# Optimization experiments

Measured on AMD Instinct MI355X. Metric: run time of the kernel, lower is better.

The kernel has to match this reference:

```python
import jax, jax.numpy as jnp
import numpy as np


def setup_inputs() -> dict:
    key = jax.random.key(0)
    ks = jax.random.split(key, 8)
    B, L, F, H, A = 128, 196, 2048, 512, 512
    features = jax.random.normal(ks[0], (B, L, F), dtype=jnp.float32)
    hidden_state = jax.random.normal(ks[1], (B, H), dtype=jnp.float32)
    # Linear params (PyTorch layout: weight [out, in], bias [out]); scaled like kaiming-uniform
    W_enc = jax.random.normal(ks[2], (A, F), dtype=jnp.float32) / np.sqrt(F)
    b_enc = jnp.zeros((A,), dtype=jnp.float32)
    W_dec = jax.random.normal(ks[3], (A, H), dtype=jnp.float32) / np.sqrt(H)
    b_dec = jnp.zeros((A,), dtype=jnp.float32)
    W_com = jax.random.normal(ks[4], (1, A), dtype=jnp.float32) / np.sqrt(A)
    b_com = jnp.zeros((1,), dtype=jnp.float32)
    return {
        "features": features, "hidden_state": hidden_state,
        "W_enc": W_enc, "b_enc": b_enc,
        "W_dec": W_dec, "b_dec": b_dec,
        "W_com": W_com, "b_com": b_com,
    }


def reference(features, hidden_state, W_enc, b_enc, W_dec, b_dec, W_com, b_com):
    # encoder_context: [B, L, A]
    enc = jnp.einsum('blf,af->bla', features, W_enc) + b_enc
    # decoder_context: [B, 1, A]
    dec = (hidden_state @ W_dec.T + b_dec)[:, None, :]
    # relu + linear to scalar score (dropout in eval mode = identity): [B, L]
    scores = jnp.einsum('bla,a->bl', jax.nn.relu(enc + dec), W_com[0]) + b_com[0]
    alpha = jax.nn.softmax(scores, axis=1)  # [B, L]
    weighted_features = jnp.einsum('blf,bl->bf', features, alpha)  # [B, F]
    return weighted_features, alpha
```

## Files before the change

### kernel.cpp

```cpp
#include <hip/hip_runtime.h>
#include <hip/hip_bf16.h>
#include <math.h>

#define B_  128
#define L_  196
#define F_  2048
#define H_  512
#define A_  512
#define ML_ (B_*L_)

typedef _Float16 half8 __attribute__((ext_vector_type(8)));
typedef _Float16 half4v __attribute__((ext_vector_type(4)));
typedef float f32x4 __attribute__((ext_vector_type(4)));

__device__ __forceinline__ void gld_lds16(const void* g, void* l) {
  __builtin_amdgcn_global_load_lds((const __attribute__((address_space(1))) void*)g,
                                   (__attribute__((address_space(3))) void*)l, 16, 0, 0);
}

__global__ __launch_bounds__(256) void k_dec(const float* __restrict__ hs,
                                             const float* __restrict__ Wdec,
                                             const float* __restrict__ bdec,
                                             const float* __restrict__ benc,
                                             float* __restrict__ dec,
                                             float* __restrict__ scores) {
  const int b = blockIdx.x, t = threadIdx.x;
  const int g = b * 256 + t;
  if (g < ML_) scores[g] = 0.f;

  __shared__ float h[H_];
  h[t]       = hs[b * H_ + t];
  h[t + 256] = hs[b * H_ + t + 256];
  __syncthreads();

#pragma unroll
  for (int r = 0; r < 2; r++) {
    const int a = t + r * 256;
    float acc = bdec[a] + benc[a];
    const float4* wr = (const float4*)(Wdec + (size_t)a * H_);
#pragma unroll 4
    for (int k4 = 0; k4 < H_ / 4; k4++) {
      const float4 w = wr[k4];
      acc += w.x * h[4*k4] + w.y * h[4*k4+1] + w.z * h[4*k4+2] + w.w * h[4*k4+3];
    }
    dec[b * A_ + a] = acc;
  }
}

__global__ __launch_bounds__(256) void k_cvt(const float4* __restrict__ src,
                                             half4v* __restrict__ dst, int n4) {
  for (int i = blockIdx.x * 256 + threadIdx.x; i < n4; i += gridDim.x * 256) {
    const float4 v = src[i];
    half4v o = { (_Float16)v.x, (_Float16)v.y, (_Float16)v.z, (_Float16)v.w };
    dst[i] = o;
  }
}

__global__ __launch_bounds__(256) void k_scores_mfma(const _Float16* __restrict__ fA,
                                                     const _Float16* __restrict__ fB,
                                                     const float* __restrict__ dec,
                                                     const float* __restrict__ wcom,
                                                     float* __restrict__ scores) {
  __shared__ _Float16 As[128 * 64];
  __shared__ _Float16 Bs[128 * 64];
  __shared__ float decS[2][128];

  const int tid  = threadIdx.x;
  const int lane = tid & 63;
  const int w    = tid >> 6;
  const int a0   = blockIdx.x * 128;
  const int m0   = blockIdx.y * 128;
  const int wm   = w & 1;
  const int wn   = w >> 1;
  const int quad = lane >> 4;
  const int l16  = lane & 15;

  f32x4 acc[4][4];
#pragma unroll
  for (int i = 0; i < 4; i++)
#pragma unroll
    for (int j = 0; j < 4; j++)
#pragma unroll
      for (int k = 0; k < 4; k++) acc[i][j][k] = 0.f;

  const int srow   = lane >> 3;
  const int schunk = (lane & 7) ^ srow;
  const _Float16* gAb = fA + (size_t)(m0 + srow) * F_ + schunk * 8;
  const _Float16* gBb = fB + (size_t)(a0 + srow) * F_ + schunk * 8;

  for (int kt = 0; kt < F_; kt += 64) {
#pragma unroll
    for (int i = 0; i < 4; i++) {
      const int r = w * 32 + i * 8;
      gld_lds16(gAb + (size_t)r * F_ + kt, &As[r * 64]);
      gld_lds16(gBb + (size_t)r * F_ + kt, &Bs[r * 64]);
    }
    __syncthreads();

#pragma unroll
    for (int k32 = 0; k32 < 2; k32++) {
      half8 af[4], bf[4];
#pragma unroll
      for (int mt = 0; mt < 4; mt++) {
        const int row = wm * 64 + mt * 16 + l16;
        const int pos = (k32 * 4 + quad) ^ (row & 7);
        af[mt] = *(const half8*)&As[row * 64 + pos * 8];
      }
#pragma unroll
      for (int at = 0; at < 4; at++) {
        const int row = wn * 64 + at * 16 + l16;
        const int pos = (k32 * 4 + quad) ^ (row & 7);
        bf[at] = *(const half8*)&Bs[row * 64 + pos * 8];
      }
#pragma unroll
      for (int mt = 0; mt < 4; mt++)
#pragma unroll
        for (int at = 0; at < 4; at++)
          acc[mt][at] = __builtin_amdgcn_mfma_f32_16x16x32_f16(af[mt], bf[at], acc[mt][at], 0, 0, 0);
    }
    __syncthreads();
  }

  const int b0 = m0 / L_;
  {
    const int i = tid >> 7;
    const int j = tid & 127;
    int bb = b0 + i; if (bb > B_ - 1) bb = B_ - 1;
    decS[i][j] = dec[bb * A_ + a0 + j];
  }
  __syncthreads();

  float w4[4];
#pragma unroll
  for (int at = 0; at < 4; at++) w4[at] = wcom[a0 + wn * 64 + at * 16 + l16];

#pragma unroll
  for (int mt = 0; mt < 4; mt++) {
#pragma unroll
    for (int r = 0; r < 4; r++) {
      const int m  = m0 + wm * 64 + mt * 16 + quad * 4 + r;
      const int db = m / L_ - b0;
      float p = 0.f;
#pragma unroll
      for (int at = 0; at < 4; at++) {
        const float e = acc[mt][at][r] + decS[db][wn * 64 + at * 16 + l16];
        p = fmaf(fmaxf(e, 0.f), w4[at], p);
      }
      p += __shfl_xor(p, 1);
      p += __shfl_xor(p, 2);
      p += __shfl_xor(p, 4);
      p += __shfl_xor(p, 8);
      if (l16 == 0) atomicAdd(&scores[m], p);
    }
  }
}

__global__ __launch_bounds__(256) void k_scores(const float* __restrict__ feat,
                                                const float* __restrict__ Wenc,
                                                const float* __restrict__ dec,
                                                const float* __restrict__ wcom,
                                                float* __restrict__ scores) {
  __shared__ float As[16][128];
  __shared__ float Bs[16][128];

  const int tid = threadIdx.x;
  const int m0 = blockIdx.x * 128;
  const int a0 = blockIdx.y * 128;
  const int tx = tid & 15;
  const int ty = tid >> 4;

  float acc[8][8];
#pragma unroll
  for (int i = 0; i < 8; i++)
#pragma unroll
    for (int j = 0; j < 8; j++) acc[i][j] = 0.f;

  for (int kt = 0; kt < F_; kt += 16) {
#pragma unroll
    for (int rep = 0; rep < 2; rep++) {
      const int idx = rep * 256 + tid;
      const int row = idx >> 2;
      const int kp  = (idx & 3) << 2;
      const float4 v = *(const float4*)(feat + (size_t)(m0 + row) * F_ + kt + kp);
      As[kp+0][row] = v.x; As[kp+1][row] = v.y; As[kp+2][row] = v.z; As[kp+3][row] = v.w;
      const float4 w = *(const float4*)(Wenc + (size_t)(a0 + row) * F_ + kt + kp);
      Bs[kp+0][row] = w.x; Bs[kp+1][row] = w.y; Bs[kp+2][row] = w.z; Bs[kp+3][row] = w.w;
    }
    __syncthreads();

#pragma unroll
    for (int k = 0; k < 16; k++) {
      float ar[8], br[8];
      *(float4*)&ar[0] = *(const float4*)&As[k][ty * 8];
      *(float4*)&ar[4] = *(const float4*)&As[k][ty * 8 + 4];
      *(float4*)&br[0] = *(const float4*)&Bs[k][tx * 8];
      *(float4*)&br[4] = *(const float4*)&Bs[k][tx * 8 + 4];
#pragma unroll
      for (int i = 0; i < 8; i++)
#pragma unroll
        for (int j = 0; j < 8; j++) acc[i][j] = fmaf(ar[i], br[j], acc[i][j]);
    }
    __syncthreads();
  }

  float w8[8];
  *(float4*)&w8[0] = *(const float4*)(wcom + a0 + tx * 8);
  *(float4*)&w8[4] = *(const float4*)(wcom + a0 + tx * 8 + 4);

#pragma unroll
  for (int i = 0; i < 8; i++) {
    const int m = m0 + ty * 8 + i;
    const int b = m / L_;
    const float* dp = dec + b * A_ + a0 + tx * 8;
    float p = 0.f;
#pragma unroll
    for (int j = 0; j < 8; j++) {
      const float e = acc[i][j] + dp[j];
      p = fmaf(fmaxf(e, 0.f), w8[j], p);
    }
    p += __shfl_xor(p, 1);
    p += __shfl_xor(p, 2);
    p += __shfl_xor(p, 4);
    p += __shfl_xor(p, 8);
    if (tx == 0) atomicAdd(&scores[m], p);
  }
}

__global__ __launch_bounds__(256) void k_softmax(const float* __restrict__ scores,
                                                 float* __restrict__ alpha) {
  const int b = blockIdx.x, t = threadIdx.x;
  __shared__ float redm[4];
  __shared__ float reds[4];

  float s = (t < L_) ? scores[b * L_ + t] : -INFINITY;

  float m = s;
#pragma unroll
  for (int o = 32; o >= 1; o >>= 1) m = fmaxf(m, __shfl_xor(m, o));
  if ((t & 63) == 0) redm[t >> 6] = m;
  __syncthreads();
  m = fmaxf(fmaxf(redm[0], redm[1]), fmaxf(redm[2], redm[3]));

  float e = (t < L_) ? expf(s - m) : 0.f;
  float sum = e;
#pragma unroll
  for (int o = 32; o >= 1; o >>= 1) sum += __shfl_xor(sum, o);
  if ((t & 63) == 0) reds[t >> 6] = sum;
  __syncthreads();
  sum = reds[0] + reds[1] + reds[2] + reds[3];

  if (t < L_) alpha[b * L_ + t] = e / sum;
}

__global__ __launch_bounds__(256) void k_wsum(const float* __restrict__ feat,
                                              const float* __restrict__ alpha,
                                              float* __restrict__ out) {
  const int fc = blockIdx.x;
  const int b  = blockIdx.y;
  const int t  = threadIdx.x;

  __shared__ float al[L_];
  for (int i = t; i < L_; i += 256) al[i] = alpha[b * L_ + i];
  __syncthreads();

  const int f = fc * 256 + t;
  const float* fp = feat + (size_t)b * L_ * F_ + f;
  float acc = 0.f;
#pragma unroll 4
  for (int l = 0; l < L_; l++) acc = fmaf(fp[(size_t)l * F_], al[l], acc);
  out[b * F_ + f] = acc;
}

extern "C" void kernel_launch(void* const* d_in, const int* in_sizes, int n_in,
                              void* d_out, int out_size, void* d_ws, size_t ws_size,
                              hipStream_t stream) {
  const float* feat = (const float*)d_in[0];
  const float* hs   = (const float*)d_in[1];
  const float* Wenc = (const float*)d_in[2];
  const float* benc = (const float*)d_in[3];
  const float* Wdec = (const float*)d_in[4];
  const float* bdec = (const float*)d_in[5];
  const float* wcom = (const float*)d_in[6];

  float* out   = (float*)d_out;
  float* alpha = out + B_ * F_;
  float* dec    = (float*)d_ws;
  float* scores = dec + B_ * A_;

  const size_t need = (size_t)(B_ * A_ + ML_) * 4
                    + ((size_t)ML_ * F_ + (size_t)A_ * F_) * 2;

  k_dec<<<dim3(B_), dim3(256), 0, stream>>>(hs, Wdec, bdec, benc, dec, scores);

  if (ws_size >= need) {
    _Float16* fH = (_Float16*)(scores + ML_);
    _Float16* wH = fH + (size_t)ML_ * F_;
    k_cvt<<<dim3(4096), dim3(256), 0, stream>>>((const float4*)feat, (half4v*)fH, ML_ * F_ / 4);
    k_cvt<<<dim3(256),  dim3(256), 0, stream>>>((const float4*)Wenc, (half4v*)wH, A_ * F_ / 4);
    k_scores_mfma<<<dim3(A_ / 128, ML_ / 128), dim3(256), 0, stream>>>(fH, wH, dec, wcom, scores);
  } else {
    k_scores<<<dim3(ML_ / 128, A_ / 128), dim3(256), 0, stream>>>(feat, Wenc, dec, wcom, scores);
  }

  k_softmax<<<dim3(B_), dim3(256), 0, stream>>>(scores, alpha);
  k_wsum<<<dim3(F_ / 256, B_), dim3(256), 0, stream>>>(feat, alpha, out);
}
```

Measured before the change: 470.4 us.

## Fuse prep kernels, fuse softmax into weighted sum, read fp16 features

The two conversion kernels and the decoder projection are merged into one launch, which removes launch gaps. Softmax is folded into the weighted-sum kernel, and each block recomputes it per batch row. The weighted sum now reads the fp16 copy of the features instead of the fp32 original, which halves that read traffic but makes the output depend on fp16-rounded inputs. The dec tile load in the MFMA kernel is moved ahead of the main loop. The weighted-sum blocks also change from 256 to 512 columns, using 2-wide loads.

```diff
diff --git a/kernel.cpp b/kernel.cpp
--- a/kernel.cpp
+++ b/kernel.cpp
@@ -11,6 +11,7 @@
 
 typedef _Float16 half8 __attribute__((ext_vector_type(8)));
 typedef _Float16 half4v __attribute__((ext_vector_type(4)));
+typedef _Float16 half2v __attribute__((ext_vector_type(2)));
 typedef float f32x4 __attribute__((ext_vector_type(4)));
 
 __device__ __forceinline__ void gld_lds16(const void* g, void* l) {
@@ -18,17 +19,39 @@
                                    (__attribute__((address_space(3))) void*)l, 16, 0, 0);
 }
 
-__global__ __launch_bounds__(256) void k_dec(const float* __restrict__ hs,
-                                             const float* __restrict__ Wdec,
-                                             const float* __restrict__ bdec,
-                                             const float* __restrict__ benc,
-                                             float* __restrict__ dec,
-                                             float* __restrict__ scores) {
-  const int b = blockIdx.x, t = threadIdx.x;
+__global__ __launch_bounds__(256) void k_prep(const float4* __restrict__ feat4,
+                                              half4v* __restrict__ fH,
+                                              const float4* __restrict__ Wenc4,
+                                              half4v* __restrict__ wH,
+                                              const float* __restrict__ hs,
+                                              const float* __restrict__ Wdec,
+                                              const float* __restrict__ bdec,
+                                              const float* __restrict__ benc,
+                                              float* __restrict__ dec,
+                                              float* __restrict__ scores) {
+  __shared__ float h[H_];
+  const int bx = blockIdx.x, t = threadIdx.x;
+
+  if (bx < 4096) {
+    const int n4 = ML_ * F_ / 4;
+    for (int i = bx * 256 + t; i < n4; i += 4096 * 256) {
+      const float4 v = feat4[i];
+      half4v o = { (_Float16)v.x, (_Float16)v.y, (_Float16)v.z, (_Float16)v.w };
+      fH[i] = o;
+    }
+    return;
+  }
+
+  const int b = bx - 4096;
   const int g = b * 256 + t;
   if (g < ML_) scores[g] = 0.f;
 
-  __shared__ float h[H_];
+  for (int i = b * 256 + t; i < A_ * F_ / 4; i += 128 * 256) {
+    const float4 v = Wenc4[i];
+    half4v o = { (_Float16)v.x, (_Float16)v.y, (_Float16)v.z, (_Float16)v.w };
+    wH[i] = o;
+  }
+
   h[t]       = hs[b * H_ + t];
   h[t + 256] = hs[b * H_ + t + 256];
   __syncthreads();
@@ -44,15 +67,6 @@
       acc += w.x * h[4*k4] + w.y * h[4*k4+1] + w.z * h[4*k4+2] + w.w * h[4*k4+3];
     }
     dec[b * A_ + a] = acc;
-  }
-}
-
-__global__ __launch_bounds__(256) void k_cvt(const float4* __restrict__ src,
-                                             half4v* __restrict__ dst, int n4) {
-  for (int i = blockIdx.x * 256 + threadIdx.x; i < n4; i += gridDim.x * 256) {
-    const float4 v = src[i];
-    half4v o = { (_Float16)v.x, (_Float16)v.y, (_Float16)v.z, (_Float16)v.w };
-    dst[i] = o;
   }
 }
 
@@ -83,44 +97,6 @@
 #pragma unroll
       for (int k = 0; k < 4; k++) acc[i][j][k] = 0.f;
 
-  const int srow   = lane >> 3;
-  const int schunk = (lane & 7) ^ srow;
-  const _Float16* gAb = fA + (size_t)(m0 + srow) * F_ + schunk * 8;
-  const _Float16* gBb = fB + (size_t)(a0 + srow) * F_ + schunk * 8;
-
-  for (int kt = 0; kt < F_; kt += 64) {
-#pragma unroll
-    for (int i = 0; i < 4; i++) {
-      const int r = w * 32 + i * 8;
-      gld_lds16(gAb + (size_t)r * F_ + kt, &As[r * 64]);
-      gld_lds16(gBb + (size_t)r * F_ + kt, &Bs[r * 64]);
-    }
-    __syncthreads();
-
-#pragma unroll
-    for (int k32 = 0; k32 < 2; k32++) {
-      half8 af[4], bf[4];
-#pragma unroll
-      for (int mt = 0; mt < 4; mt++) {
-        const int row = wm * 64 + mt * 16 + l16;
-        const int pos = (k32 * 4 + quad) ^ (row & 7);
-        af[mt] = *(const half8*)&As[row * 64 + pos * 8];
-      }
-#pragma unroll
-      for (int at = 0; at < 4; at++) {
-        const int row = wn * 64 + at * 16 + l16;
-        const int pos = (k32 * 4 + quad) ^ (row & 7);
-        bf[at] = *(const half8*)&Bs[row * 64 + pos * 8];
-      }
-#pragma unroll
-      for (int mt = 0; mt < 4; mt++)
-#pragma unroll
-        for (int at = 0; at < 4; at++)
-          acc[mt][at] = __builtin_amdgcn_mfma_f32_16x16x32_f16(af[mt], bf[at], acc[mt][at], 0, 0, 0);
-    }
-    __syncthreads();
-  }
-
   const int b0 = m0 / L_;
   {
     const int i = tid >> 7;
@@ -128,7 +104,44 @@
     int bb = b0 + i; if (bb > B_ - 1) bb = B_ - 1;
     decS[i][j] = dec[bb * A_ + a0 + j];
   }
-  __syncthreads();
+
+  const int srow   = lane >> 3;
+  const int schunk = (lane & 7) ^ srow;
+  const _Float16* gAb = fA + (size_t)(m0 + srow) * F_ + schunk * 8;
+  const _Float16* gBb = fB + (size_t)(a0 + srow) * F_ + schunk * 8;
+
+  for (int kt = 0; kt < F_; kt += 64) {
+#pragma unroll
+    for (int i = 0; i < 4; i++) {
+      const int r = w * 32 + i * 8;
+      gld_lds16(gAb + (size_t)r * F_ + kt, &As[r * 64]);
+      gld_lds16(gBb + (size_t)r * F_ + kt, &Bs[r * 64]);
+    }
+    __syncthreads();
+
+#pragma unroll
+    for (int k32 = 0; k32 < 2; k32++) {
+      half8 af[4], bf[4];
+#pragma unroll
+      for (int mt = 0; mt < 4; mt++) {
+        const int row = wm * 64 + mt * 16 + l16;
+        const int pos = (k32 * 4 + quad) ^ (row & 7);
+        af[mt] = *(const half8*)&As[row * 64 + pos * 8];
+      }
+#pragma unroll
+      for (int at = 0; at < 4; at++) {
+        const int row = wn * 64 + at * 16 + l16;
+        const int pos = (k32 * 4 + quad) ^ (row & 7);
+        bf[at] = *(const half8*)&Bs[row * 64 + pos * 8];
+      }
+#pragma unroll
+      for (int mt = 0; mt < 4; mt++)
+#pragma unroll
+        for (int at = 0; at < 4; at++)
+          acc[mt][at] = __builtin_amdgcn_mfma_f32_16x16x32_f16(af[mt], bf[at], acc[mt][at], 0, 0, 0);
+    }
+    __syncthreads();
+  }
 
   float w4[4];
 #pragma unroll
@@ -155,6 +168,53 @@
   }
 }
 
+__global__ __launch_bounds__(256) void k_attn(const _Float16* __restrict__ fH,
+                                              const float* __restrict__ scores,
+                                              float* __restrict__ alpha,
+                                              float* __restrict__ out) {
+  const int fc = blockIdx.x, b = blockIdx.y, t = threadIdx.x;
+  __shared__ float al[L_];
+  __shared__ float redm[4];
+  __shared__ float reds[4];
+
+  float s = (t < L_) ? scores[b * L_ + t] : -INFINITY;
+
+  float m = s;
+#pragma unroll
+  for (int o = 32; o >= 1; o >>= 1) m = fmaxf(m, __shfl_xor(m, o));
+  if ((t & 63) == 0) redm[t >> 6] = m;
+  __syncthreads();
+  m = fmaxf(fmaxf(redm[0], redm[1]), fmaxf(redm[2], redm[3]));
+
+  float e = (t < L_) ? expf(s - m) : 0.f;
+  float sum = e;
+#pragma unroll
+  for (int o = 32; o >= 1; o >>= 1) sum += __shfl_xor(sum, o);
+  if ((t & 63) == 0) reds[t >> 6] = sum;
+  __syncthreads();
+  sum = reds[0] + reds[1] + reds[2] + reds[3];
+
+  if (t < L_) {
+    const float a = e / sum;
+    al[t] = a;
+    if (fc == 0) alpha[b * L_ + t] = a;
+  }
+  __syncthreads();
+
+  const int f0 = fc * 512 + t * 2;
+  const half2v* fp = (const half2v*)(fH + (size_t)b * L_ * F_ + f0);
+  float ax = 0.f, ay = 0.f;
+#pragma unroll 4
+  for (int l = 0; l < L_; l++) {
+    const half2v v = fp[(size_t)l * (F_ / 2)];
+    const float w = al[l];
+    ax = fmaf((float)v.x, w, ax);
+    ay = fmaf((float)v.y, w, ay);
+  }
+  float2 o = { ax, ay };
+  *(float2*)(out + (size_t)b * F_ + f0) = o;
+}
+
 __global__ __launch_bounds__(256) void k_scores(const float* __restrict__ feat,
                                                 const float* __restrict__ Wenc,
                                                 const float* __restrict__ dec,
@@ -226,21 +286,22 @@
   }
 }
 
-__global__ __launch_bounds__(256) void k_softmax(const float* __restrict__ scores,
-                                                 float* __restrict__ alpha) {
-  const int b = blockIdx.x, t = threadIdx.x;
+__global__ __launch_bounds__(256) void k_attn_f32(const float* __restrict__ feat,
+                                                  const float* __restrict__ scores,
+                                                  float* __restrict__ alpha,
+                                                  float* __restrict__ out) {
+  const int fc = blockIdx.x, b = blockIdx.y, t = threadIdx.x;
+  __shared__ float al[L_];
   __shared__ float redm[4];
   __shared__ float reds[4];
 
   float s = (t < L_) ? scores[b * L_ + t] : -INFINITY;
-
   float m = s;
 #pragma unroll
   for (int o = 32; o >= 1; o >>= 1) m = fmaxf(m, __shfl_xor(m, o));
   if ((t & 63) == 0) redm[t >> 6] = m;
   __syncthreads();
   m = fmaxf(fmaxf(redm[0], redm[1]), fmaxf(redm[2], redm[3]));
-
   float e = (t < L_) ? expf(s - m) : 0.f;
   float sum = e;
 #pragma unroll
@@ -248,27 +309,52 @@
   if ((t & 63) == 0) reds[t >> 6] = sum;
   __syncthreads();
   sum = reds[0] + reds[1] + reds[2] + reds[3];
-
-  if (t < L_) alpha[b * L_ + t] = e / sum;
-}
-
-__global__ __launch_bounds__(256) void k_wsum(const float* __restrict__ feat,
-                                              const float* __restrict__ alpha,
-                                              float* __restrict__ out) {
-  const int fc = blockIdx.x;
-  const int b  = blockIdx.y;
-  const int t  = threadIdx.x;
-
-  __shared__ float al[L_];
-  for (int i = t; i < L_; i += 256) al[i] = alpha[b * L_ + i];
-  __syncthreads();
-
-  const int f = fc * 256 + t;
-  const float* fp = feat + (size_t)b * L_ * F_ + f;
-  float acc = 0.f;
+  if (t < L_) {
+    const float a = e / sum;
+    al[t] = a;
+    if (fc == 0) alpha[b * L_ + t] = a;
+  }
+  __syncthreads();
+
+  const int f0 = fc * 512 + t * 2;
+  const float2* fp = (const float2*)(feat + (size_t)b * L_ * F_ + f0);
+  float ax = 0.f, ay = 0.f;
 #pragma unroll 4
-  for (int l = 0; l < L_; l++) acc = fmaf(fp[(size_t)l * F_], al[l], acc);
-  out[b * F_ + f] = acc;
+  for (int l = 0; l < L_; l++) {
+    const float2 v = fp[(size_t)l * (F_ / 2)];
+    const float w = al[l];
+    ax = fmaf(v.x, w, ax);
+    ay = fmaf(v.y, w, ay);
+  }
+  float2 o = { ax, ay };
+  *(float2*)(out + (size_t)b * F_ + f0) = o;
+}
+
+__global__ __launch_bounds__(256) void k_dec_only(const float* __restrict__ hs,
+                                                  const float* __restrict__ Wdec,
+                                                  const float* __restrict__ bdec,
+                                                  const float* __restrict__ benc,
+                                                  float* __restrict__ dec,
+                                                  float* __restrict__ scores) {
+  const int b = blockIdx.x, t = threadIdx.x;
+  const int g = b * 256 + t;
+  if (g < ML_) scores[g] = 0.f;
+  __shared__ float h[H_];
+  h[t]       = hs[b * H_ + t];
+  h[t + 256] = hs[b * H_ + t + 256];
+  __syncthreads();
+#pragma unroll
+  for (int r = 0; r < 2; r++) {
+    const int a = t + r * 256;
+    float acc = bdec[a] + benc[a];
+    const float4* wr = (const float4*)(Wdec + (size_t)a * H_);
+#pragma unroll 4
+    for (int k4 = 0; k4 < H_ / 4; k4++) {
+      const float4 w = wr[k4];
+      acc += w.x * h[4*k4] + w.y * h[4*k4+1] + w.z * h[4*k4+2] + w.w * h[4*k4+3];
+    }
+    dec[b * A_ + a] = acc;
+  }
 }
 
 extern "C" void kernel_launch(void* const* d_in, const int* in_sizes, int n_in,
@@ -290,18 +376,17 @@
   const size_t need = (size_t)(B_ * A_ + ML_) * 4
                     + ((size_t)ML_ * F_ + (size_t)A_ * F_) * 2;
 
-  k_dec<<<dim3(B_), dim3(256), 0, stream>>>(hs, Wdec, bdec, benc, dec, scores);
-
   if (ws_size >= need) {
     _Float16* fH = (_Float16*)(scores + ML_);
     _Float16* wH = fH + (size_t)ML_ * F_;
-    k_cvt<<<dim3(4096), dim3(256), 0, stream>>>((const float4*)feat, (half4v*)fH, ML_ * F_ / 4);
-    k_cvt<<<dim3(256),  dim3(256), 0, stream>>>((const float4*)Wenc, (half4v*)wH, A_ * F_ / 4);
+    k_prep<<<dim3(4096 + 128), dim3(256), 0, stream>>>(
+        (const float4*)feat, (half4v*)fH, (const float4*)Wenc, (half4v*)wH,
+        hs, Wdec, bdec, benc, dec, scores);
     k_scores_mfma<<<dim3(A_ / 128, ML_ / 128), dim3(256), 0, stream>>>(fH, wH, dec, wcom, scores);
+    k_attn<<<dim3(4, B_), dim3(256), 0, stream>>>(fH, scores, alpha, out);
   } else {
+    k_dec_only<<<dim3(B_), dim3(256), 0, stream>>>(hs, Wdec, bdec, benc, dec, scores);
     k_scores<<<dim3(ML_ / 128, A_ / 128), dim3(256), 0, stream>>>(feat, Wenc, dec, wcom, scores);
-  }
-
-  k_softmax<<<dim3(B_), dim3(256), 0, stream>>>(scores, alpha);
-  k_wsum<<<dim3(F_ / 256, B_), dim3(256), 0, stream>>>(feat, alpha, out);
-}
+    k_attn_f32<<<dim3(4, B_), dim3(256), 0, stream>>>(feat, scores, alpha, out);
+  }
+}
```

After: 502.7 us. 1.07x slower.
